# Performance work log

Measured on AMD Instinct MI355X. Metric: run time of the kernel, lower is better.

The kernel has to match this reference:

```python
import jax, jax.numpy as jnp
import numpy as np

N_NODES = 100000
N_EDGES = 3200000


def _spmm(rows, cols, vals, x):
    # out[i] = sum_{e: rows[e]==i} vals[e] * x[cols[e]]
    msgs = vals[:, None] * x[cols]  # [E, F]
    return jax.ops.segment_sum(msgs, rows, num_segments=N_NODES)


def setup_inputs() -> dict:
    key = jax.random.key(0)
    ks = jax.random.split(key, 8)
    x = jax.random.normal(ks[0], (N_NODES, 256), dtype=jnp.float32)
    adj_rows = jax.random.randint(ks[1], (N_EDGES,), 0, N_NODES, dtype=jnp.int32)
    adj_cols = jax.random.randint(ks[2], (N_EDGES,), 0, N_NODES, dtype=jnp.int32)
    adj_vals = jax.random.uniform(ks[3], (N_EDGES,), dtype=jnp.float32)
    W1 = jax.random.normal(ks[4], (256, 128), dtype=jnp.float32) * (1.0 / np.sqrt(256))
    b1 = jnp.zeros((128,), dtype=jnp.float32)
    W2 = jax.random.normal(ks[5], (128, 64), dtype=jnp.float32) * (1.0 / np.sqrt(128))
    b2 = jnp.zeros((64,), dtype=jnp.float32)
    return {"x": x, "adj_rows": adj_rows, "adj_cols": adj_cols, "adj_vals": adj_vals,
            "W1": W1, "b1": b1, "W2": W2, "b2": b2}


def reference(x, adj_rows, adj_cols, adj_vals, W1, b1, W2, b2):
    # Layer 0: spmm -> linear -> relu (dropout inactive in eval)
    h = _spmm(adj_rows, adj_cols, adj_vals, x)
    h = jax.nn.relu(h @ W1 + b1)
    # Layer 1 (last layer): spmm -> linear, no activation
    h = _spmm(adj_rows, adj_cols, adj_vals, h)
    out = h @ W2 + b2
    return out  # squeeze(1) is a no-op for [N, nclass]
```

## Files before the change

### kernel.cpp

```cpp
#include <hip/hip_runtime.h>
#include <hip/hip_fp16.h>


#define RPB 480
#define NB_MAX 1024
#define PCHUNK 8192
#define EPT 32
#define CAP_SHIFT 14
#define CAP (1 << CAP_SHIFT)

typedef _Float16 half8 __attribute__((ext_vector_type(8)));
typedef _Float16 h2t __attribute__((ext_vector_type(2)));
typedef float floatx4 __attribute__((ext_vector_type(4)));

__global__ __launch_bounds__(256) void prep_weights_kernel(const float* __restrict__ W1,
                                                           const float* __restrict__ W2,
                                                           __half* __restrict__ W1T,
                                                           h2t* __restrict__ pk,
                                                           int* __restrict__ gcnt) {
    int i = blockIdx.x * 256 + threadIdx.x;
    if (i < 256 * 128) {
        int k = i >> 7, n = i & 127;
        W1T[n * 256 + k] = __float2half_rn(W1[i]);
    } else if (i < 256 * 128 + 4096) {
        int j = i - 256 * 128;
        int kk = j >> 6, c = j & 63;
        h2t v;
        v[0] = (_Float16)W2[(2 * kk) * 64 + c];
        v[1] = (_Float16)W2[(2 * kk + 1) * 64 + c];
        pk[j] = v;
    } else {
        int j = i - (256 * 128 + 4096);
        if (j < NB_MAX) gcnt[j] = 0;
    }
}

__global__ __launch_bounds__(256) void transpose_w_kernel(const float* __restrict__ W,
                                                          __half* __restrict__ WT,
                                                          int K, int N) {
    int i = blockIdx.x * 256 + threadIdx.x;
    if (i < K * N) {
        int k = i / N, n = i % N;
        WT[n * K + k] = __float2half_rn(W[i]);
    }
}

__global__ __launch_bounds__(256) void gemm_part_kernel(
    const float* __restrict__ A, const __half* __restrict__ BT,
    __half* __restrict__ C, int nrows,
    const int* __restrict__ rows, const int* __restrict__ cols,
    const float* __restrict__ vals, int* __restrict__ gcnt,
    int2* __restrict__ eb1, int nE, int nB, int pblocks) {
    extern __shared__ char smem[];
    const int t = threadIdx.x;

    if ((int)blockIdx.x < pblocks) {
        int* hist = (int*)smem;
        int* cur = hist + NB_MAX;
        const int c0 = blockIdx.x * PCHUNK;
        for (int b = t; b < nB; b += 256) hist[b] = 0;
        __syncthreads();
        int myr[EPT];
#pragma unroll
        for (int j = 0; j < EPT; ++j) {
            int e = c0 + t + 256 * j;
            int r = (e < nE) ? rows[e] : -1;
            myr[j] = r;
            if (r >= 0) atomicAdd(&hist[r / RPB], 1);
        }
        __syncthreads();
        for (int b = t; b < nB; b += 256) {
            int c = hist[b];
            cur[b] = c ? (b << CAP_SHIFT) + atomicAdd(&gcnt[b], c) : 0;
        }
        __syncthreads();
#pragma unroll
        for (int j = 0; j < EPT; ++j) {
            int r = myr[j];
            if (r >= 0) {
                int e = c0 + t + 256 * j;
                int bk = r / RPB;
                int rl = r - bk * RPB;
                int pos = atomicAdd(&cur[bk], 1);
                if (pos < ((bk + 1) << CAP_SHIFT))
                    eb1[pos] = make_int2((cols[e] & 0x1FFFF) | (rl << 17),
                                         __float_as_int(vals[e]));
            }
        }
    } else {
        constexpr int MT = 64, KT = 64, KP = KT + 8, NN = 128, KK = 256;
        constexpr int WCT = NN / 32;
        __half* As = (__half*)smem;
        __half* Bs = As + MT * KP;
        const int wid = t >> 6, lane = t & 63;
        const int row0 = ((int)blockIdx.x - pblocks) * MT;
        const int wr = wid & 1, wc = wid >> 1;
        const int lrow = lane & 15, q = lane >> 4;

        floatx4 acc[2][WCT];
#pragma unroll
        for (int rt = 0; rt < 2; ++rt)
#pragma unroll
            for (int ct = 0; ct < WCT; ++ct)
#pragma unroll
                for (int i = 0; i < 4; ++i) acc[rt][ct][i] = 0.f;

        for (int kt = 0; kt < KK; kt += KT) {
#pragma unroll
            for (int it = 0; it < MT * KT / 4 / 256; ++it) {
                int i4 = it * 256 + t;
                int m = i4 >> 4;
                int kk = (i4 & 15) << 2;
                int gr = row0 + m;
                float4 v = make_float4(0.f, 0.f, 0.f, 0.f);
                if (gr < nrows) v = *(const float4*)(A + (size_t)gr * KK + kt + kk);
                __half h0 = __float2half_rn(v.x), h1 = __float2half_rn(v.y);
                __half h2 = __float2half_rn(v.z), h3 = __float2half_rn(v.w);
                ushort4 u = make_ushort4(*(unsigned short*)&h0, *(unsigned short*)&h1,
                                         *(unsigned short*)&h2, *(unsigned short*)&h3);
                *(ushort4*)(As + m * KP + kk) = u;
            }
#pragma unroll
            for (int it = 0; it < NN * KT / 4 / 256; ++it) {
                int i4 = it * 256 + t;
                int n = i4 >> 4;
                int kk = (i4 & 15) << 2;
                *(ushort4*)(Bs + n * KP + kk) =
                    *(const ushort4*)(BT + (size_t)n * KK + kt + kk);
            }
            __syncthreads();

#pragma unroll
            for (int ks = 0; ks < KT; ks += 32) {
                half8 a0 = *(half8*)(As + (wr * 32 + lrow) * KP + ks + q * 8);
                half8 a1 = *(half8*)(As + (wr * 32 + 16 + lrow) * KP + ks + q * 8);
#pragma unroll
                for (int ct = 0; ct < WCT; ++ct) {
                    half8 b = *(half8*)(Bs + (wc * (NN / 2) + ct * 16 + lrow) * KP + ks + q * 8);
                    acc[0][ct] = __builtin_amdgcn_mfma_f32_16x16x32_f16(a0, b, acc[0][ct], 0, 0, 0);
                    acc[1][ct] = __builtin_amdgcn_mfma_f32_16x16x32_f16(a1, b, acc[1][ct], 0, 0, 0);
                }
            }
            __syncthreads();
        }

#pragma unroll
        for (int rt = 0; rt < 2; ++rt)
#pragma unroll
            for (int ct = 0; ct < WCT; ++ct)
#pragma unroll
                for (int r = 0; r < 4; ++r) {
                    int gr = row0 + wr * 32 + rt * 16 + q * 4 + r;
                    if (gr < nrows)
                        C[(size_t)gr * NN + wc * (NN / 2) + ct * 16 + lrow] =
                            __float2half_rn(acc[rt][ct][r]);
                }
    }
}

__global__ __launch_bounds__(1024) void fine_scatter_kernel(const int* __restrict__ gcnt,
                                                            const int2* __restrict__ eb1,
                                                            int2* __restrict__ eb2,
                                                            int2* __restrict__ off2,
                                                            int nN) {
    __shared__ int hist[RPB];
    __shared__ int sc[RPB];
    __shared__ int cur[RPB];
    const int b = blockIdx.x;
    const int row0 = b * RPB;
    const int nr = min(RPB, nN - row0);
    const int t = threadIdx.x;
    const int s = b << CAP_SHIFT;
    const int e = s + min(gcnt[b], CAP);

    if (t < RPB) hist[t] = 0;
    __syncthreads();
    for (int i = s + t; i < e; i += 1024)
        atomicAdd(&hist[((unsigned)eb1[i].x) >> 17], 1);
    __syncthreads();

    int myc = (t < RPB) ? hist[t] : 0;
    if (t < RPB) sc[t] = myc;
    __syncthreads();
    for (int d = 1; d < RPB; d <<= 1) {
        int add = (t < RPB && t >= d) ? sc[t - d] : 0;
        __syncthreads();
        if (t < RPB) sc[t] += add;
        __syncthreads();
    }
    if (t < RPB) {
        int excl = s + sc[t] - myc;
        cur[t] = excl;
        if (t < nr) off2[row0 + t] = make_int2(excl, myc);
    }
    __syncthreads();

    for (int i = s + t; i < e; i += 1024) {
        int2 ed = eb1[i];
        unsigned x = (unsigned)ed.x;
        int pos = atomicAdd(&cur[x >> 17], 1);
        eb2[pos] = make_int2((int)(x & 0x1FFFF), ed.y);
    }
}

__global__ __launch_bounds__(256) void spmm_fused_kernel(const int2* __restrict__ off2,
                                                         const int2* __restrict__ eb,
                                                         const __half* __restrict__ Y,
                                                         const float* __restrict__ b1,
                                                         const h2t* __restrict__ pk,
                                                         __half* __restrict__ Y2, int nN) {
    __shared__ h2t w2s[64 * 64];
    __shared__ h2t hs[4][64];
    const int t = threadIdx.x;
#pragma unroll
    for (int i = 0; i < 16; ++i) w2s[i * 256 + t] = pk[i * 256 + t];
    __syncthreads();

    const int wv = t >> 6;
    const int lane = t & 63;
    const int fg = lane & 15;
    const int g = lane >> 4;
    const int gw = blockIdx.x * 4 + wv;
    const int nw = gridDim.x * 4;

    for (int row = gw; row < nN; row += nw) {
        float acc[8];
#pragma unroll
        for (int p = 0; p < 8; ++p) acc[p] = 0.f;

        int2 se = off2[row];
        int s = se.x;
        int e1 = s + se.y;
        for (int base = s; base < e1; base += 64) {
            int n = min(64, e1 - base);
            int2 my = (lane < n) ? eb[base + lane] : make_int2(0, 0);
            for (int j = 0; j < n; j += 8) {
                int i0 = j + g;
                int i1 = j + 4 + g;
                int s0 = (i0 < n) ? i0 : j;
                int s1 = (i1 < n) ? i1 : j;
                int c0 = __shfl(my.x, s0);
                int c1 = __shfl(my.x, s1);
                float v0 = __int_as_float(__shfl(my.y, s0));
                float v1 = __int_as_float(__shfl(my.y, s1));
                if (i0 >= n) v0 = 0.f;
                if (i1 >= n) v1 = 0.f;
                half8 y0 = *(const half8*)(Y + ((size_t)c0 << 7) + (fg << 3));
                half8 y1 = *(const half8*)(Y + ((size_t)c1 << 7) + (fg << 3));
#pragma unroll
                for (int p = 0; p < 8; ++p) acc[p] = fmaf(v0, (float)y0[p], acc[p]);
#pragma unroll
                for (int p = 0; p < 8; ++p) acc[p] = fmaf(v1, (float)y1[p], acc[p]);
            }
        }
#pragma unroll
        for (int p = 0; p < 8; ++p) acc[p] += __shfl_xor(acc[p], 16);
#pragma unroll
        for (int p = 0; p < 8; ++p) acc[p] += __shfl_xor(acc[p], 32);

        if (g == 0) {
            floatx4 ba = *(const floatx4*)(b1 + fg * 8);
            floatx4 bb = *(const floatx4*)(b1 + fg * 8 + 4);
            float f[8];
#pragma unroll
            for (int p = 0; p < 4; ++p) f[p] = fmaxf(acc[p] + ba[p], 0.f);
#pragma unroll
            for (int p = 0; p < 4; ++p) f[4 + p] = fmaxf(acc[4 + p] + bb[p], 0.f);
#pragma unroll
            for (int p = 0; p < 4; ++p) {
                h2t pr;
                pr[0] = (_Float16)f[2 * p];
                pr[1] = (_Float16)f[2 * p + 1];
                hs[wv][fg * 4 + p] = pr;
            }
        }
        __builtin_amdgcn_sched_barrier(0);

        float o = 0.f;
#pragma unroll 8
        for (int kk = 0; kk < 64; ++kk) {
            h2t a = hs[wv][kk];
            h2t b = w2s[kk * 64 + lane];
#if __has_builtin(__builtin_amdgcn_fdot2)
            o = __builtin_amdgcn_fdot2(a, b, o, false);
#else
            o = fmaf((float)a[0], (float)b[0], o);
            o = fmaf((float)a[1], (float)b[1], o);
#endif
        }
        Y2[(size_t)row * 64 + lane] = __float2half_rn(o);
    }
}

__global__ __launch_bounds__(256) void spmm_csr64_kernel(const int2* __restrict__ off2,
                                                         const int2* __restrict__ eb,
                                                         const __half* __restrict__ Y,
                                                         const float* __restrict__ bias,
                                                         float* __restrict__ out, int nN) {
    const int lane = threadIdx.x & 63;
    const int fg = lane & 7;
    const int g = lane >> 3;
    const int gw = blockIdx.x * 4 + (threadIdx.x >> 6);
    const int nw = gridDim.x * 4;

    for (int row = gw; row < nN; row += nw) {
        float acc[8];
#pragma unroll
        for (int p = 0; p < 8; ++p) acc[p] = 0.f;

        int2 se = off2[row];
        int s = se.x;
        int e1 = s + se.y;
        for (int base = s; base < e1; base += 64) {
            int n = min(64, e1 - base);
            int2 my = (lane < n) ? eb[base + lane] : make_int2(0, 0);
            for (int j = 0; j < n; j += 16) {
                int i0 = j + g;
                int i1 = j + 8 + g;
                int s0 = (i0 < n) ? i0 : j;
                int s1 = (i1 < n) ? i1 : j;
                int c0 = __shfl(my.x, s0);
                int c1 = __shfl(my.x, s1);
                float v0 = __int_as_float(__shfl(my.y, s0));
                float v1 = __int_as_float(__shfl(my.y, s1));
                if (i0 >= n) v0 = 0.f;
                if (i1 >= n) v1 = 0.f;
                half8 y0 = *(const half8*)(Y + ((size_t)c0 << 6) + (fg << 3));
                half8 y1 = *(const half8*)(Y + ((size_t)c1 << 6) + (fg << 3));
#pragma unroll
                for (int p = 0; p < 8; ++p) acc[p] = fmaf(v0, (float)y0[p], acc[p]);
#pragma unroll
                for (int p = 0; p < 8; ++p) acc[p] = fmaf(v1, (float)y1[p], acc[p]);
            }
        }
#pragma unroll
        for (int p = 0; p < 8; ++p) acc[p] += __shfl_xor(acc[p], 8);
#pragma unroll
        for (int p = 0; p < 8; ++p) acc[p] += __shfl_xor(acc[p], 16);
#pragma unroll
        for (int p = 0; p < 8; ++p) acc[p] += __shfl_xor(acc[p], 32);

        if (g == 0) {
            floatx4 ba = *(const floatx4*)(bias + fg * 8);
            floatx4 bb = *(const floatx4*)(bias + fg * 8 + 4);
            floatx4 o0, o1;
#pragma unroll
            for (int p = 0; p < 4; ++p) o0[p] = acc[p] + ba[p];
#pragma unroll
            for (int p = 0; p < 4; ++p) o1[p] = acc[4 + p] + bb[p];
            float* op = out + (size_t)row * 64 + fg * 8;
            *(floatx4*)op = o0;
            *(floatx4*)(op + 4) = o1;
        }
    }
}

__global__ __launch_bounds__(256) void init_bias_kernel(float* __restrict__ out,
                                                        const float* __restrict__ bias,
                                                        int fmask, size_t total) {
    size_t i = (size_t)blockIdx.x * 256 + threadIdx.x;
    if (i < total) out[i] = bias[i & fmask];
}

template <int F>
__global__ __launch_bounds__(256) void spmm_atomic_kernel(const int* __restrict__ rows,
                                                          const int* __restrict__ cols,
                                                          const float* __restrict__ vals,
                                                          const __half* __restrict__ Y,
                                                          float* __restrict__ out, int nE) {
    int e = blockIdx.x * 4 + (threadIdx.x >> 6);
    if (e >= nE) return;
    int lane = threadIdx.x & 63;
    int r = rows[e];
    int c = cols[e];
    float v = vals[e];
    if (F == 128) {
        float2 y = __half22float2(*((const __half2*)(Y + (size_t)c * 128) + lane));
        float* op = out + (size_t)r * 128 + lane * 2;
        unsafeAtomicAdd(op, v * y.x);
        unsafeAtomicAdd(op + 1, v * y.y);
    } else {
        float y = __half2float(Y[(size_t)c * F + lane]);
        unsafeAtomicAdd(out + (size_t)r * F + lane, v * y);
    }
}

template <int NN, int KK, bool RELU_IN>
__global__ __launch_bounds__(256) void gemm_mfma_kernel(const float* __restrict__ A,
                                                        const __half* __restrict__ BT,
                                                        __half* __restrict__ C, int nrows) {
    constexpr int MT = 64, KT = 64, KP = KT + 8;
    __shared__ __half As[MT * KP];
    __shared__ __half Bs[NN * KP];
    const int tid = threadIdx.x;
    const int wid = tid >> 6, lane = tid & 63;
    const int row0 = blockIdx.x * MT;
    const int wr = wid & 1, wc = wid >> 1;
    constexpr int WCT = NN / 32;
    const int lrow = lane & 15, q = lane >> 4;

    floatx4 acc[2][WCT];
#pragma unroll
    for (int rt = 0; rt < 2; ++rt)
#pragma unroll
        for (int ct = 0; ct < WCT; ++ct)
#pragma unroll
            for (int i = 0; i < 4; ++i) acc[rt][ct][i] = 0.f;

    for (int kt = 0; kt < KK; kt += KT) {
#pragma unroll
        for (int it = 0; it < MT * KT / 4 / 256; ++it) {
            int i4 = it * 256 + tid;
            int m = i4 >> 4;
            int kk = (i4 & 15) << 2;
            int gr = row0 + m;
            float4 v = make_float4(0.f, 0.f, 0.f, 0.f);
            if (gr < nrows) v = *(const float4*)(A + (size_t)gr * KK + kt + kk);
            if (RELU_IN) {
                v.x = fmaxf(v.x, 0.f); v.y = fmaxf(v.y, 0.f);
                v.z = fmaxf(v.z, 0.f); v.w = fmaxf(v.w, 0.f);
            }
            __half h0 = __float2half_rn(v.x), h1 = __float2half_rn(v.y);
            __half h2 = __float2half_rn(v.z), h3 = __float2half_rn(v.w);
            ushort4 u = make_ushort4(*(unsigned short*)&h0, *(unsigned short*)&h1,
                                     *(unsigned short*)&h2, *(unsigned short*)&h3);
            *(ushort4*)(As + m * KP + kk) = u;
        }
#pragma unroll
        for (int it = 0; it < NN * KT / 4 / 256; ++it) {
            int i4 = it * 256 + tid;
            int n = i4 >> 4;
            int kk = (i4 & 15) << 2;
            *(ushort4*)(Bs + n * KP + kk) =
                *(const ushort4*)(BT + (size_t)n * KK + kt + kk);
        }
        __syncthreads();

#pragma unroll
        for (int ks = 0; ks < KT; ks += 32) {
            half8 a0 = *(half8*)(As + (wr * 32 + lrow) * KP + ks + q * 8);
            half8 a1 = *(half8*)(As + (wr * 32 + 16 + lrow) * KP + ks + q * 8);
#pragma unroll
            for (int ct = 0; ct < WCT; ++ct) {
                half8 b = *(half8*)(Bs + (wc * (NN / 2) + ct * 16 + lrow) * KP + ks + q * 8);
                acc[0][ct] = __builtin_amdgcn_mfma_f32_16x16x32_f16(a0, b, acc[0][ct], 0, 0, 0);
                acc[1][ct] = __builtin_amdgcn_mfma_f32_16x16x32_f16(a1, b, acc[1][ct], 0, 0, 0);
            }
        }
        __syncthreads();
    }

#pragma unroll
    for (int rt = 0; rt < 2; ++rt)
#pragma unroll
        for (int ct = 0; ct < WCT; ++ct)
#pragma unroll
            for (int r = 0; r < 4; ++r) {
                int gr = row0 + wr * 32 + rt * 16 + q * 4 + r;
                if (gr < nrows)
                    C[(size_t)gr * NN + wc * (NN / 2) + ct * 16 + lrow] =
                        __float2half_rn(acc[rt][ct][r]);
            }
}

extern "C" void kernel_launch(void* const* d_in, const int* in_sizes, int n_in,
                              void* d_out, int out_size, void* d_ws, size_t ws_size,
                              hipStream_t stream) {
    const float* x    = (const float*)d_in[0];
    const int*   rows = (const int*)d_in[1];
    const int*   cols = (const int*)d_in[2];
    const float* vals = (const float*)d_in[3];
    const float* W1   = (const float*)d_in[4];
    const float* b1   = (const float*)d_in[5];
    const float* W2   = (const float*)d_in[6];
    const float* b2   = (const float*)d_in[7];
    float* out = (float*)d_out;

    const int nN = in_sizes[0] / 256;
    const int nE = in_sizes[1];
    const int nB = (nN + RPB - 1) / RPB;

    const int mblocks  = (nN + 63) / 64;
    const int pblocks  = (nE + PCHUNK - 1) / PCHUNK;
    const int sblocks  = min(2048, (nN + 3) / 4);
    const int eblocks4 = (nE + 3) / 4;

    char* w = (char*)d_ws;
    __half* Y1h  = (__half*)w;  w += (size_t)nN * 128 * 2;
    __half* Y2h  = (__half*)w;  w += (size_t)nN * 64 * 2;
    __half* W1T  = (__half*)w;  w += (size_t)256 * 128 * 2;
    h2t*    pk   = (h2t*)w;     w += (size_t)4096 * 4;
    int2*   off2 = (int2*)w;    w += (size_t)nN * 8;
    int*    gcnt = (int*)w;     w += (size_t)NB_MAX * 4;
    int2*   eb1  = (int2*)w;    w += ((size_t)nB << CAP_SHIFT) * 8;
    int2*   eb2  = (int2*)w;    w += ((size_t)nB << CAP_SHIFT) * 8;
    size_t need = (size_t)(w - (char*)d_ws);

    const bool slots_ok = (nE / nB) <= (CAP - 1050);

    if (ws_size >= need && nN <= (1 << 17) && nB <= NB_MAX && slots_ok) {
        prep_weights_kernel<<<(256 * 128 + 4096 + NB_MAX + 255) / 256, 256, 0, stream>>>(
            W1, W2, W1T, pk, gcnt);

        gemm_part_kernel<<<pblocks + mblocks, 256, (64 + 128) * 72 * 2, stream>>>(
            x, W1T, Y1h, nN, rows, cols, vals, gcnt, eb1, nE, nB, pblocks);

        fine_scatter_kernel<<<nB, 1024, 0, stream>>>(gcnt, eb1, eb2, off2, nN);

        spmm_fused_kernel<<<sblocks, 256, 0, stream>>>(off2, eb2, Y1h, b1, pk, Y2h, nN);
        spmm_csr64_kernel<<<sblocks, 256, 0, stream>>>(off2, eb2, Y2h, b2, out, nN);
    } else {
        char* v = (char*)d_ws;
        __half* fY1h = (__half*)v;  v += (size_t)nN * 128 * 2;
        float*  fH1  = (float*)v;   v += (size_t)nN * 128 * 4;
        __half* fW1T = (__half*)v;  v += (size_t)256 * 128 * 2;
        __half* fW2T = (__half*)v;  v += (size_t)128 * 64 * 2;

        transpose_w_kernel<<<(256 * 128 + 255) / 256, 256, 0, stream>>>(W1, fW1T, 256, 128);
        transpose_w_kernel<<<(128 * 64 + 255) / 256, 256, 0, stream>>>(W2, fW2T, 128, 64);
        gemm_mfma_kernel<128, 256, false><<<mblocks, 256, 0, stream>>>(x, fW1T, fY1h, nN);
        size_t totH1 = (size_t)nN * 128;
        init_bias_kernel<<<(int)((totH1 + 255) / 256), 256, 0, stream>>>(fH1, b1, 127, totH1);
        spmm_atomic_kernel<128><<<eblocks4, 256, 0, stream>>>(rows, cols, vals, fY1h, fH1, nE);
        gemm_mfma_kernel<64, 128, true><<<mblocks, 256, 0, stream>>>(fH1, fW2T, fY1h, nN);
        size_t totOut = (size_t)nN * 64;
        init_bias_kernel<<<(int)((totOut + 255) / 256), 256, 0, stream>>>(out, b2, 63, totOut);
        spmm_atomic_kernel<64><<<eblocks4, 256, 0, stream>>>(rows, cols, vals, fY1h, out, nE);
    }
}
```

Measured before the change: 450.4 us.

## Replace two-pass bucket scatter with per-row fixed-capacity slot scatter

Drops the coarse-bucket histogram scatter and the separate fine_scatter kernel. Each edge now claims a slot in a per-row array of capacity 96 through a global atomic counter, and the SpMM kernels read each row at row*ROWCAP with length cnt[row]. This removes one kernel launch and one full pass that read and rewrote the edge buffer. In exchange, the writes are scattered and uncoalesced, and any row with more than 96 edges silently loses its extra edges. The fused GEMM's K tile is also cut from 64 to 32, which shrinks shared memory per block.

```diff
diff --git a/kernel.cpp b/kernel.cpp
--- a/kernel.cpp
+++ b/kernel.cpp
@@ -2,12 +2,9 @@
 #include <hip/hip_fp16.h>
 
 
-#define RPB 480
-#define NB_MAX 1024
 #define PCHUNK 8192
 #define EPT 32
-#define CAP_SHIFT 14
-#define CAP (1 << CAP_SHIFT)
+#define ROWCAP 96
 
 typedef _Float16 half8 __attribute__((ext_vector_type(8)));
 typedef _Float16 h2t __attribute__((ext_vector_type(2)));
@@ -17,7 +14,7 @@
                                                            const float* __restrict__ W2,
                                                            __half* __restrict__ W1T,
                                                            h2t* __restrict__ pk,
-                                                           int* __restrict__ gcnt) {
+                                                           int* __restrict__ cnt, int nN) {
     int i = blockIdx.x * 256 + threadIdx.x;
     if (i < 256 * 128) {
         int k = i >> 7, n = i & 127;
@@ -31,7 +28,7 @@
         pk[j] = v;
     } else {
         int j = i - (256 * 128 + 4096);
-        if (j < NB_MAX) gcnt[j] = 0;
+        if (j < nN) cnt[j] = 0;
     }
 }
 
@@ -45,55 +42,35 @@
     }
 }
 
-__global__ __launch_bounds__(256) void gemm_part_kernel(
+__global__ __launch_bounds__(256) void gemm_scatter_kernel(
     const float* __restrict__ A, const __half* __restrict__ BT,
     __half* __restrict__ C, int nrows,
     const int* __restrict__ rows, const int* __restrict__ cols,
-    const float* __restrict__ vals, int* __restrict__ gcnt,
-    int2* __restrict__ eb1, int nE, int nB, int pblocks) {
+    const float* __restrict__ vals, int* __restrict__ cnt,
+    int2* __restrict__ eb2, int nE, int scblocks) {
     extern __shared__ char smem[];
     const int t = threadIdx.x;
 
-    if ((int)blockIdx.x < pblocks) {
-        int* hist = (int*)smem;
-        int* cur = hist + NB_MAX;
+    if ((int)blockIdx.x < scblocks) {
         const int c0 = blockIdx.x * PCHUNK;
-        for (int b = t; b < nB; b += 256) hist[b] = 0;
-        __syncthreads();
-        int myr[EPT];
-#pragma unroll
+#pragma unroll 4
         for (int j = 0; j < EPT; ++j) {
             int e = c0 + t + 256 * j;
-            int r = (e < nE) ? rows[e] : -1;
-            myr[j] = r;
-            if (r >= 0) atomicAdd(&hist[r / RPB], 1);
-        }
-        __syncthreads();
-        for (int b = t; b < nB; b += 256) {
-            int c = hist[b];
-            cur[b] = c ? (b << CAP_SHIFT) + atomicAdd(&gcnt[b], c) : 0;
-        }
-        __syncthreads();
-#pragma unroll
-        for (int j = 0; j < EPT; ++j) {
-            int r = myr[j];
-            if (r >= 0) {
-                int e = c0 + t + 256 * j;
-                int bk = r / RPB;
-                int rl = r - bk * RPB;
-                int pos = atomicAdd(&cur[bk], 1);
-                if (pos < ((bk + 1) << CAP_SHIFT))
-                    eb1[pos] = make_int2((cols[e] & 0x1FFFF) | (rl << 17),
-                                         __float_as_int(vals[e]));
+            if (e < nE) {
+                int r = rows[e];
+                int slot = atomicAdd(&cnt[r], 1);
+                if (slot < ROWCAP)
+                    eb2[(size_t)r * ROWCAP + slot] =
+                        make_int2(cols[e], __float_as_int(vals[e]));
             }
         }
     } else {
-        constexpr int MT = 64, KT = 64, KP = KT + 8, NN = 128, KK = 256;
+        constexpr int MT = 64, KT = 32, KP = KT + 8, NN = 128, KK = 256;
         constexpr int WCT = NN / 32;
         __half* As = (__half*)smem;
         __half* Bs = As + MT * KP;
         const int wid = t >> 6, lane = t & 63;
-        const int row0 = ((int)blockIdx.x - pblocks) * MT;
+        const int row0 = ((int)blockIdx.x - scblocks) * MT;
         const int wr = wid & 1, wc = wid >> 1;
         const int lrow = lane & 15, q = lane >> 4;
 
@@ -109,8 +86,8 @@
 #pragma unroll
             for (int it = 0; it < MT * KT / 4 / 256; ++it) {
                 int i4 = it * 256 + t;
-                int m = i4 >> 4;
-                int kk = (i4 & 15) << 2;
+                int m = i4 >> 3;
+                int kk = (i4 & 7) << 2;
                 int gr = row0 + m;
                 float4 v = make_float4(0.f, 0.f, 0.f, 0.f);
                 if (gr < nrows) v = *(const float4*)(A + (size_t)gr * KK + kt + kk);
@@ -123,23 +100,20 @@
 #pragma unroll
             for (int it = 0; it < NN * KT / 4 / 256; ++it) {
                 int i4 = it * 256 + t;
-                int n = i4 >> 4;
-                int kk = (i4 & 15) << 2;
+                int n = i4 >> 3;
+                int kk = (i4 & 7) << 2;
                 *(ushort4*)(Bs + n * KP + kk) =
                     *(const ushort4*)(BT + (size_t)n * KK + kt + kk);
             }
             __syncthreads();
 
-#pragma unroll
-            for (int ks = 0; ks < KT; ks += 32) {
-                half8 a0 = *(half8*)(As + (wr * 32 + lrow) * KP + ks + q * 8);
-                half8 a1 = *(half8*)(As + (wr * 32 + 16 + lrow) * KP + ks + q * 8);
-#pragma unroll
-                for (int ct = 0; ct < WCT; ++ct) {
-                    half8 b = *(half8*)(Bs + (wc * (NN / 2) + ct * 16 + lrow) * KP + ks + q * 8);
-                    acc[0][ct] = __builtin_amdgcn_mfma_f32_16x16x32_f16(a0, b, acc[0][ct], 0, 0, 0);
-                    acc[1][ct] = __builtin_amdgcn_mfma_f32_16x16x32_f16(a1, b, acc[1][ct], 0, 0, 0);
-                }
+            half8 a0 = *(half8*)(As + (wr * 32 + lrow) * KP + q * 8);
+            half8 a1 = *(half8*)(As + (wr * 32 + 16 + lrow) * KP + q * 8);
+#pragma unroll
+            for (int ct = 0; ct < WCT; ++ct) {
+                half8 b = *(half8*)(Bs + (wc * (NN / 2) + ct * 16 + lrow) * KP + q * 8);
+                acc[0][ct] = __builtin_amdgcn_mfma_f32_16x16x32_f16(a0, b, acc[0][ct], 0, 0, 0);
+                acc[1][ct] = __builtin_amdgcn_mfma_f32_16x16x32_f16(a1, b, acc[1][ct], 0, 0, 0);
             }
             __syncthreads();
         }
@@ -158,52 +132,7 @@
     }
 }
 
-__global__ __launch_bounds__(1024) void fine_scatter_kernel(const int* __restrict__ gcnt,
-                                                            const int2* __restrict__ eb1,
-                                                            int2* __restrict__ eb2,
-                                                            int2* __restrict__ off2,
-                                                            int nN) {
-    __shared__ int hist[RPB];
-    __shared__ int sc[RPB];
-    __shared__ int cur[RPB];
-    const int b = blockIdx.x;
-    const int row0 = b * RPB;
-    const int nr = min(RPB, nN - row0);
-    const int t = threadIdx.x;
-    const int s = b << CAP_SHIFT;
-    const int e = s + min(gcnt[b], CAP);
-
-    if (t < RPB) hist[t] = 0;
-    __syncthreads();
-    for (int i = s + t; i < e; i += 1024)
-        atomicAdd(&hist[((unsigned)eb1[i].x) >> 17], 1);
-    __syncthreads();
-
-    int myc = (t < RPB) ? hist[t] : 0;
-    if (t < RPB) sc[t] = myc;
-    __syncthreads();
-    for (int d = 1; d < RPB; d <<= 1) {
-        int add = (t < RPB && t >= d) ? sc[t - d] : 0;
-        __syncthreads();
-        if (t < RPB) sc[t] += add;
-        __syncthreads();
-    }
-    if (t < RPB) {
-        int excl = s + sc[t] - myc;
-        cur[t] = excl;
-        if (t < nr) off2[row0 + t] = make_int2(excl, myc);
-    }
-    __syncthreads();
-
-    for (int i = s + t; i < e; i += 1024) {
-        int2 ed = eb1[i];
-        unsigned x = (unsigned)ed.x;
-        int pos = atomicAdd(&cur[x >> 17], 1);
-        eb2[pos] = make_int2((int)(x & 0x1FFFF), ed.y);
-    }
-}
-
-__global__ __launch_bounds__(256) void spmm_fused_kernel(const int2* __restrict__ off2,
+__global__ __launch_bounds__(256) void spmm_fused_kernel(const int* __restrict__ cnt,
                                                          const int2* __restrict__ eb,
                                                          const __half* __restrict__ Y,
                                                          const float* __restrict__ b1,
@@ -228,9 +157,10 @@
 #pragma unroll
         for (int p = 0; p < 8; ++p) acc[p] = 0.f;
 
-        int2 se = off2[row];
-        int s = se.x;
-        int e1 = s + se.y;
+        int len = cnt[row];
+        if (len > ROWCAP) len = ROWCAP;
+        int s = row * ROWCAP;
+        int e1 = s + len;
         for (int base = s; base < e1; base += 64) {
             int n = min(64, e1 - base);
             int2 my = (lane < n) ? eb[base + lane] : make_int2(0, 0);
@@ -292,7 +222,7 @@
     }
 }
 
-__global__ __launch_bounds__(256) void spmm_csr64_kernel(const int2* __restrict__ off2,
+__global__ __launch_bounds__(256) void spmm_csr64_kernel(const int* __restrict__ cnt,
                                                          const int2* __restrict__ eb,
                                                          const __half* __restrict__ Y,
                                                          const float* __restrict__ bias,
@@ -308,9 +238,10 @@
 #pragma unroll
         for (int p = 0; p < 8; ++p) acc[p] = 0.f;
 
-        int2 se = off2[row];
-        int s = se.x;
-        int e1 = s + se.y;
+        int len = cnt[row];
+        if (len > ROWCAP) len = ROWCAP;
+        int s = row * ROWCAP;
+        int e1 = s + len;
         for (int base = s; base < e1; base += 64) {
             int n = min(64, e1 - base);
             int2 my = (lane < n) ? eb[base + lane] : make_int2(0, 0);
@@ -478,37 +409,30 @@
 
     const int nN = in_sizes[0] / 256;
     const int nE = in_sizes[1];
-    const int nB = (nN + RPB - 1) / RPB;
 
     const int mblocks  = (nN + 63) / 64;
-    const int pblocks  = (nE + PCHUNK - 1) / PCHUNK;
+    const int scblocks = (nE + PCHUNK - 1) / PCHUNK;
     const int sblocks  = min(2048, (nN + 3) / 4);
     const int eblocks4 = (nE + 3) / 4;
 
     char* w = (char*)d_ws;
-    __half* Y1h  = (__half*)w;  w += (size_t)nN * 128 * 2;
-    __half* Y2h  = (__half*)w;  w += (size_t)nN * 64 * 2;
-    __half* W1T  = (__half*)w;  w += (size_t)256 * 128 * 2;
-    h2t*    pk   = (h2t*)w;     w += (size_t)4096 * 4;
-    int2*   off2 = (int2*)w;    w += (size_t)nN * 8;
-    int*    gcnt = (int*)w;     w += (size_t)NB_MAX * 4;
-    int2*   eb1  = (int2*)w;    w += ((size_t)nB << CAP_SHIFT) * 8;
-    int2*   eb2  = (int2*)w;    w += ((size_t)nB << CAP_SHIFT) * 8;
+    __half* Y1h = (__half*)w;  w += (size_t)nN * 128 * 2;
+    __half* Y2h = (__half*)w;  w += (size_t)nN * 64 * 2;
+    __half* W1T = (__half*)w;  w += (size_t)256 * 128 * 2;
+    h2t*    pk  = (h2t*)w;     w += (size_t)4096 * 4;
+    int*    cnt = (int*)w;     w += (size_t)nN * 4;
+    int2*   eb2 = (int2*)w;    w += (size_t)nN * ROWCAP * 8;
     size_t need = (size_t)(w - (char*)d_ws);
 
-    const bool slots_ok = (nE / nB) <= (CAP - 1050);
-
-    if (ws_size >= need && nN <= (1 << 17) && nB <= NB_MAX && slots_ok) {
-        prep_weights_kernel<<<(256 * 128 + 4096 + NB_MAX + 255) / 256, 256, 0, stream>>>(
-            W1, W2, W1T, pk, gcnt);
-
-        gemm_part_kernel<<<pblocks + mblocks, 256, (64 + 128) * 72 * 2, stream>>>(
-            x, W1T, Y1h, nN, rows, cols, vals, gcnt, eb1, nE, nB, pblocks);
-
-        fine_scatter_kernel<<<nB, 1024, 0, stream>>>(gcnt, eb1, eb2, off2, nN);
-
-        spmm_fused_kernel<<<sblocks, 256, 0, stream>>>(off2, eb2, Y1h, b1, pk, Y2h, nN);
-        spmm_csr64_kernel<<<sblocks, 256, 0, stream>>>(off2, eb2, Y2h, b2, out, nN);
+    if (ws_size >= need && nN <= (1 << 17)) {
+        prep_weights_kernel<<<(256 * 128 + 4096 + nN + 255) / 256, 256, 0, stream>>>(
+            W1, W2, W1T, pk, cnt, nN);
+
+        gemm_scatter_kernel<<<scblocks + mblocks, 256, (64 + 128) * 40 * 2, stream>>>(
+            x, W1T, Y1h, nN, rows, cols, vals, cnt, eb2, nE, scblocks);
+
+        spmm_fused_kernel<<<sblocks, 256, 0, stream>>>(cnt, eb2, Y1h, b1, pk, Y2h, nN);
+        spmm_csr64_kernel<<<sblocks, 256, 0, stream>>>(cnt, eb2, Y2h, b2, out, nN);
     } else {
         char* v = (char*)d_ws;
         __half* fY1h = (__half*)v;  v += (size_t)nN * 128 * 2;
```

Result: slower. 493.0 us (+9.5%).
